# Kernel optimization log

Hardware: AMD Instinct MI355X
Metric: run time of the kernel (lower is better)

The kernel has to match this reference:

```python
import jax, jax.numpy as jnp
import numpy as np
import math

N, KZ, IFZ, AHZ, AFZ = 20000, 16, 256, 8, 32
EPS = 1e-5


def layernorm(x, g, b):
    m = jnp.mean(x, axis=-1, keepdims=True)
    v = jnp.mean((x - m) ** 2, axis=-1, keepdims=True)
    return (x - m) * jax.lax.rsqrt(v + EPS) * g + b


def rotate_half(x):
    x1, x2 = jnp.split(x, 2, axis=-1)
    return jnp.concatenate([-x2, x1], axis=-1)


def setup_inputs() -> dict:
    key = jax.random.key(0)
    ks = jax.random.split(key, 16)
    s = 1.0 / math.sqrt(IFZ)
    hf = AHZ * AFZ
    return {
        "x_1": jax.random.normal(ks[0], (N, IFZ), jnp.float32),
        "x_2": jax.random.normal(ks[1], (N, KZ, IFZ), jnp.float32),
        "pos_emb": jax.random.normal(ks[2], (N, AFZ), jnp.float32),
        "edge_index": jax.random.randint(ks[3], (N, KZ), 0, N),
        "Wq": jax.random.normal(ks[4], (IFZ, hf), jnp.float32) * s,
        "Wk": jax.random.normal(ks[5], (IFZ, hf), jnp.float32) * s,
        "Wv": jax.random.normal(ks[6], (IFZ, hf), jnp.float32) * s,
        "Wb": jax.random.normal(ks[7], (IFZ, AHZ), jnp.float32) * s,
        "bln_g": jnp.ones((IFZ,), jnp.float32),
        "bln_b": jnp.zeros((IFZ,), jnp.float32),
        "Wg": jax.random.normal(ks[8], (IFZ, hf), jnp.float32) * s,
        "bg": jnp.zeros((hf,), jnp.float32),
        "Wback": jax.random.normal(ks[9], (hf, IFZ), jnp.float32) / math.sqrt(hf),
        "bback": jnp.zeros((IFZ,), jnp.float32),
        "ln1_g": jnp.ones((IFZ,), jnp.float32),
        "ln1_b": jnp.zeros((IFZ,), jnp.float32),
    }


def reference(x_1, x_2, pos_emb, edge_index, Wq, Wk, Wv, Wb, bln_g, bln_b,
              Wg, bg, Wback, bback, ln1_g, ln1_b):
    n = x_1.shape[0]
    y_1 = x_1[edge_index]                                  # [N,kz,ifz] irregular gather
    q = (x_1 @ Wq).reshape(n, AHZ, AFZ)                    # [N,h,f]
    k = (y_1 @ Wk).reshape(n, KZ, AHZ, AFZ)                # [N,kz,h,f]
    # RoPE: rotate q by each node's own angles, k by gathered neighbor angles
    cos_q = jnp.cos(pos_emb)[:, None, :]                   # [N,1,f]
    sin_q = jnp.sin(pos_emb)[:, None, :]
    q = q * cos_q + rotate_half(q) * sin_q
    pe_n = pos_emb[edge_index]                             # [N,kz,f]
    cos_k = jnp.cos(pe_n)[:, :, None, :]                   # [N,kz,1,f]
    sin_k = jnp.sin(pe_n)[:, :, None, :]
    k = k * cos_k + rotate_half(k) * sin_k
    v = (y_1 @ Wv).reshape(n, KZ, AHZ, AFZ)
    bias_2 = layernorm(x_2, bln_g, bln_b) @ Wb             # [N,kz,h]
    gate = jax.nn.sigmoid(x_1 @ Wg + bg).reshape(n, AHZ, AFZ)
    scores = jnp.einsum('nhf,nkhf->nkh', q, k) / math.sqrt(AFZ) + bias_2
    w = jax.nn.softmax(scores, axis=1)                     # over kz neighbors
    out = gate * jnp.einsum('nkh,nkhf->nhf', w, v)         # [N,h,f]
    out = out.reshape(n, AHZ * AFZ) @ Wback + bback + math.sqrt(2.0) * x_1
    return layernorm(out, ln1_g, ln1_b)
```

## Files before the change

### kernel.cpp

```cpp
#include <hip/hip_runtime.h>
#include <math.h>

#define IFZ 256
#define KZ  16
#define AHZ 8
#define AFZ 32
#define HF  256

typedef _Float16 half8 __attribute__((ext_vector_type(8)));
typedef _Float16 half4 __attribute__((ext_vector_type(4)));
typedef float    f32x4 __attribute__((ext_vector_type(4)));

__global__ void conv_f16(const float* __restrict__ in, _Float16* __restrict__ out, int n4)
{
    int i = blockIdx.x * 256 + threadIdx.x;
    if (i >= n4) return;
    float4 v = reinterpret_cast<const float4*>(in)[i];
    half4 h;
    h[0] = (_Float16)v.x; h[1] = (_Float16)v.y;
    h[2] = (_Float16)v.z; h[3] = (_Float16)v.w;
    reinterpret_cast<half4*>(out)[i] = h;
}

__global__ void conv_wt(const float* __restrict__ w0, const float* __restrict__ w1,
                        const float* __restrict__ w2, const float* __restrict__ w3,
                        const float* __restrict__ w4, _Float16* __restrict__ out)
{
    int k = blockIdx.x;
    int m = blockIdx.y;
    int c = threadIdx.x;
    const float* w = (m == 0) ? w0 : (m == 1) ? w1 : (m == 2) ? w2 : (m == 3) ? w3 : w4;
    out[(size_t)m * 65536 + (size_t)c * 256 + k] = (_Float16)w[(size_t)k * 256 + c];
}

__global__ void prep_c1(const float* __restrict__ g, const float* __restrict__ b,
                        const float* __restrict__ Wb,
                        _Float16* __restrict__ c1T, float* __restrict__ c23)
{
    __shared__ float red[4][16];
    const int f = threadIdx.x;
    const int w = f >> 6, l = f & 63;
    const float gv = g[f], bv = b[f];
    float ph2[8], ph3[8];
    #pragma unroll
    for (int h = 0; h < 8; ++h) {
        float wv = Wb[(size_t)f * 8 + h];
        c1T[h * 256 + f] = (_Float16)(gv * wv);
        ph2[h] = gv * wv;
        ph3[h] = bv * wv;
    }
    c1T[8 * 256 + f] = (_Float16)1.0f;
    #pragma unroll
    for (int cc = 9; cc < 16; ++cc) c1T[cc * 256 + f] = (_Float16)0.0f;

    #pragma unroll
    for (int h = 0; h < 8; ++h) {
        #pragma unroll
        for (int o = 32; o > 0; o >>= 1) {
            ph2[h] += __shfl_xor(ph2[h], o);
            ph3[h] += __shfl_xor(ph3[h], o);
        }
        if (l == h) { red[w][h] = ph2[h]; red[w][8 + h] = ph3[h]; }
    }
    __syncthreads();
    if (f < 16) c23[f] = red[0][f] + red[1][f] + red[2][f] + red[3][f];
}

__launch_bounds__(256)
__global__ void gemm_qkvg(const _Float16* __restrict__ A, const _Float16* __restrict__ WT,
                          const float* __restrict__ pe, const float* __restrict__ bg,
                          _Float16* __restrict__ QH, _Float16* __restrict__ KH,
                          _Float16* __restrict__ VH, _Float16* __restrict__ GH, int N)
{
    __shared__ _Float16 as[64][40];
    __shared__ _Float16 bs[4][64][40];

    const int tid = threadIdx.x;
    const int l   = tid & 63;
    const int w   = tid >> 6;
    const int n0  = blockIdx.x * 64;
    const int c0  = blockIdx.y * 64;

    f32x4 acc[4][4];
    #pragma unroll
    for (int m = 0; m < 4; ++m)
        #pragma unroll
        for (int b = 0; b < 4; ++b)
            { acc[m][b][0]=0.f; acc[m][b][1]=0.f; acc[m][b][2]=0.f; acc[m][b][3]=0.f; }

    const int srow = tid >> 2;
    const int sch  = (tid & 3) * 8;
    const size_t aoff = (size_t)(n0 + srow) * IFZ + sch;
    const size_t boff = (size_t)(c0 + srow) * IFZ + sch;

    half8 av{}, bv0, bv1, bv2, bv3;
    if (n0 + srow < N) av = *reinterpret_cast<const half8*>(A + aoff);
    bv0 = *reinterpret_cast<const half8*>(WT + 0 * 65536 + boff);
    bv1 = *reinterpret_cast<const half8*>(WT + 1 * 65536 + boff);
    bv2 = *reinterpret_cast<const half8*>(WT + 2 * 65536 + boff);
    bv3 = *reinterpret_cast<const half8*>(WT + 3 * 65536 + boff);

    for (int kt = 0; kt < 8; ++kt) {
        __syncthreads();
        *reinterpret_cast<half8*>(&as[srow][sch])    = av;
        *reinterpret_cast<half8*>(&bs[0][srow][sch]) = bv0;
        *reinterpret_cast<half8*>(&bs[1][srow][sch]) = bv1;
        *reinterpret_cast<half8*>(&bs[2][srow][sch]) = bv2;
        *reinterpret_cast<half8*>(&bs[3][srow][sch]) = bv3;
        __syncthreads();

        half8 nav{}, nbv0{}, nbv1{}, nbv2{}, nbv3{};
        if (kt < 7) {
            const int k0 = (kt + 1) * 32;
            if (n0 + srow < N) nav = *reinterpret_cast<const half8*>(A + aoff + k0);
            nbv0 = *reinterpret_cast<const half8*>(WT + 0 * 65536 + boff + k0);
            nbv1 = *reinterpret_cast<const half8*>(WT + 1 * 65536 + boff + k0);
            nbv2 = *reinterpret_cast<const half8*>(WT + 2 * 65536 + boff + k0);
            nbv3 = *reinterpret_cast<const half8*>(WT + 3 * 65536 + boff + k0);
        }

        half8 af = *reinterpret_cast<const half8*>(&as[16 * w + (l & 15)][8 * (l >> 4)]);
        #pragma unroll
        for (int m = 0; m < 4; ++m) {
            #pragma unroll
            for (int b = 0; b < 4; ++b) {
                half8 bf = *reinterpret_cast<const half8*>(&bs[m][16 * b + (l & 15)][8 * (l >> 4)]);
                acc[m][b] = __builtin_amdgcn_mfma_f32_16x16x32_f16(af, bf, acc[m][b], 0, 0, 0);
            }
        }
        av = nav; bv0 = nbv0; bv1 = nbv1; bv2 = nbv2; bv3 = nbv3;
    }

    #pragma unroll
    for (int r = 0; r < 4; ++r) {
        const int grow = n0 + 16 * w + ((l >> 4) << 2) + r;
        if (grow >= N) continue;
        float a0 = pe[(size_t)grow * AFZ + (l & 15)];
        float a1 = pe[(size_t)grow * AFZ + 16 + (l & 15)];
        float s0, c0f, s1, c1f;
        __sincosf(a0, &s0, &c0f);
        __sincosf(a1, &s1, &c1f);
        #pragma unroll
        for (int m = 0; m < 2; ++m) {
            _Float16* o = m ? KH : QH;
            #pragma unroll
            for (int pb = 0; pb < 4; pb += 2) {
                float v0 = acc[m][pb][r], v1 = acc[m][pb + 1][r];
                o[(size_t)grow * HF + c0 + 16 * pb       + (l & 15)] = (_Float16)(v0 * c0f - v1 * s0);
                o[(size_t)grow * HF + c0 + 16 * (pb + 1) + (l & 15)] = (_Float16)(v1 * c1f + v0 * s1);
            }
        }
        #pragma unroll
        for (int b = 0; b < 4; ++b)
            VH[(size_t)grow * HF + c0 + 16 * b + (l & 15)] = (_Float16)acc[2][b][r];
        #pragma unroll
        for (int b = 0; b < 4; ++b) {
            const int c = c0 + 16 * b + (l & 15);
            float v = acc[3][b][r] + bg[c];
            GH[(size_t)grow * HF + c] = (_Float16)(1.f / (1.f + __expf(-v)));
        }
    }
}

__launch_bounds__(256)
__global__ void bias2_mfma(const float* __restrict__ x2,
                           const _Float16* __restrict__ c1T,
                           const float* __restrict__ c23,
                           float* __restrict__ out, int R)
{
    const int tid = threadIdx.x;
    const int l = tid & 63;
    const int w = tid >> 6;
    const int c = l & 15;
    const int p = l >> 4;

    const int R0 = (blockIdx.x * 4 + w) * 16;
    if (R0 >= R) return;

    const int arow = (R0 + c < R) ? (R0 + c) : (R - 1);
    const float* xr = x2 + (size_t)arow * IFZ + p * 8;

    f32x4 xv[16];
    #pragma unroll
    for (int kt = 0; kt < 8; ++kt) {
        xv[2 * kt]     = __builtin_nontemporal_load(reinterpret_cast<const f32x4*>(xr + kt * 32));
        xv[2 * kt + 1] = __builtin_nontemporal_load(reinterpret_cast<const f32x4*>(xr + kt * 32 + 4));
    }

    half8 bf[8];
    #pragma unroll
    for (int kt = 0; kt < 8; ++kt)
        bf[kt] = *reinterpret_cast<const half8*>(c1T + (size_t)c * 256 + kt * 32 + p * 8);

    f32x4 acc1 = {0.f, 0.f, 0.f, 0.f};
    f32x4 acc2 = {0.f, 0.f, 0.f, 0.f};
    #pragma unroll
    for (int kt = 0; kt < 8; ++kt) {
        f32x4 xa = xv[2 * kt], xb = xv[2 * kt + 1];
        half8 ax, ax2;
        ax[0] = (_Float16)xa[0]; ax[1] = (_Float16)xa[1];
        ax[2] = (_Float16)xa[2]; ax[3] = (_Float16)xa[3];
        ax[4] = (_Float16)xb[0]; ax[5] = (_Float16)xb[1];
        ax[6] = (_Float16)xb[2]; ax[7] = (_Float16)xb[3];
        ax2[0] = (_Float16)(xa[0] * xa[0]); ax2[1] = (_Float16)(xa[1] * xa[1]);
        ax2[2] = (_Float16)(xa[2] * xa[2]); ax2[3] = (_Float16)(xa[3] * xa[3]);
        ax2[4] = (_Float16)(xb[0] * xb[0]); ax2[5] = (_Float16)(xb[1] * xb[1]);
        ax2[6] = (_Float16)(xb[2] * xb[2]); ax2[7] = (_Float16)(xb[3] * xb[3]);
        acc1 = __builtin_amdgcn_mfma_f32_16x16x32_f16(ax,  bf[kt], acc1, 0, 0, 0);
        acc2 = __builtin_amdgcn_mfma_f32_16x16x32_f16(ax2, bf[kt], acc2, 0, 0, 0);
    }

    const float c2v = (c < 8) ? c23[c]     : 0.f;
    const float c3v = (c < 8) ? c23[8 + c] : 0.f;
    const int srcl = (l & 48) | 8;
    #pragma unroll
    for (int j = 0; j < 4; ++j) {
        float s1 = __shfl(acc1[j], srcl);
        float s2 = __shfl(acc2[j], srcl);
        float m    = s1 * (1.f / 256.f);
        float var  = s2 * (1.f / 256.f) - m * m;
        float rstd = rsqrtf(var + 1e-5f);
        const int row = R0 + 4 * p + j;
        if (c < 8 && row < R)
            out[(size_t)row * 8 + c] = rstd * (acc1[j] - m * c2v) + c3v;
    }
}

__launch_bounds__(256)
__global__ void attn_node(const _Float16* __restrict__ Qh, const _Float16* __restrict__ Kh,
                          const _Float16* __restrict__ Vh, const _Float16* __restrict__ Gh,
                          const int* __restrict__ eidx, const float* __restrict__ b2,
                          _Float16* __restrict__ AOh, int N)
{
    const int tid = threadIdx.x;
    const int l   = tid & 63;
    const int w   = tid >> 6;
    const int n   = blockIdx.x * 4 + w;
    if (n >= N) return;
    const int h = l >> 3;

    const int ei_reg = eidx[(size_t)n * KZ + (l & 15)];

    half4 qh4 = *reinterpret_cast<const half4*>(Qh + (size_t)n * HF + 4 * l);
    const float q0 = (float)qh4[0], q1 = (float)qh4[1],
                q2 = (float)qh4[2], q3 = (float)qh4[3];

    const float b2a = b2[(size_t)n * 128 + l];
    const float b2b = b2[(size_t)n * 128 + 64 + l];

    float sc[16];
    #pragma unroll
    for (int e = 0; e < 16; ++e) {
        const int row = __shfl(ei_reg, e);
        half4 kh4 = *reinterpret_cast<const half4*>(Kh + (size_t)row * HF + 4 * l);
        float s = q0 * (float)kh4[0] + q1 * (float)kh4[1]
                + q2 * (float)kh4[2] + q3 * (float)kh4[3];
        s += __shfl_xor(s, 1); s += __shfl_xor(s, 2); s += __shfl_xor(s, 4);
        sc[e] = s * 0.17677669529663687f;
    }
    #pragma unroll
    for (int e = 0; e < 8; ++e) sc[e]     += __shfl(b2a, e * 8 + h);
    #pragma unroll
    for (int e = 0; e < 8; ++e) sc[e + 8] += __shfl(b2b, e * 8 + h);

    float m = sc[0];
    #pragma unroll
    for (int e = 1; e < 16; ++e) m = fmaxf(m, sc[e]);
    float sum = 0.f;
    #pragma unroll
    for (int e = 0; e < 16; ++e) { sc[e] = __expf(sc[e] - m); sum += sc[e]; }
    const float inv = 1.f / sum;

    float o0 = 0.f, o1 = 0.f, o2 = 0.f, o3 = 0.f;
    #pragma unroll
    for (int e = 0; e < 16; ++e) {
        const int row = __shfl(ei_reg, e);
        half4 vh4 = *reinterpret_cast<const half4*>(Vh + (size_t)row * HF + 4 * l);
        const float we = sc[e] * inv;
        o0 = fmaf(we, (float)vh4[0], o0);
        o1 = fmaf(we, (float)vh4[1], o1);
        o2 = fmaf(we, (float)vh4[2], o2);
        o3 = fmaf(we, (float)vh4[3], o3);
    }

    half4 gh4 = *reinterpret_cast<const half4*>(Gh + (size_t)n * HF + 4 * l);
    half4 oh;
    oh[0] = (_Float16)(o0 * (float)gh4[0]);
    oh[1] = (_Float16)(o1 * (float)gh4[1]);
    oh[2] = (_Float16)(o2 * (float)gh4[2]);
    oh[3] = (_Float16)(o3 * (float)gh4[3]);
    *reinterpret_cast<half4*>(AOh + (size_t)n * HF + 4 * l) = oh;
}

__launch_bounds__(256)
__global__ void gemm_back(const _Float16* __restrict__ A, const _Float16* __restrict__ BT,
                          const float* __restrict__ bias, float* __restrict__ Y, int N)
{
    __shared__ _Float16 as[64][40];
    __shared__ _Float16 bs[64][40];

    const int tid = threadIdx.x;
    const int l   = tid & 63;
    const int w   = tid >> 6;
    const int n0  = blockIdx.x * 64;
    const int c0  = blockIdx.y * 64;

    f32x4 acc[4];
    #pragma unroll
    for (int b = 0; b < 4; ++b) { acc[b][0]=0.f; acc[b][1]=0.f; acc[b][2]=0.f; acc[b][3]=0.f; }

    const int srow = tid >> 2;
    const int sch  = (tid & 3) * 8;
    const size_t aoff = (size_t)(n0 + srow) * IFZ + sch;
    const size_t boff = (size_t)(c0 + srow) * IFZ + sch;

    half8 av{}, bv;
    if (n0 + srow < N) av = *reinterpret_cast<const half8*>(A + aoff);
    bv = *reinterpret_cast<const half8*>(BT + boff);

    for (int kt = 0; kt < 8; ++kt) {
        __syncthreads();
        *reinterpret_cast<half8*>(&as[srow][sch]) = av;
        *reinterpret_cast<half8*>(&bs[srow][sch]) = bv;
        __syncthreads();

        half8 nav{}, nbv{};
        if (kt < 7) {
            const int k0 = (kt + 1) * 32;
            if (n0 + srow < N) nav = *reinterpret_cast<const half8*>(A + aoff + k0);
            nbv = *reinterpret_cast<const half8*>(BT + boff + k0);
        }

        half8 af = *reinterpret_cast<const half8*>(&as[16 * w + (l & 15)][8 * (l >> 4)]);
        #pragma unroll
        for (int b = 0; b < 4; ++b) {
            half8 bf = *reinterpret_cast<const half8*>(&bs[16 * b + (l & 15)][8 * (l >> 4)]);
            acc[b] = __builtin_amdgcn_mfma_f32_16x16x32_f16(af, bf, acc[b], 0, 0, 0);
        }
        av = nav; bv = nbv;
    }

    #pragma unroll
    for (int r = 0; r < 4; ++r) {
        const int grow = n0 + 16 * w + ((l >> 4) << 2) + r;
        if (grow >= N) continue;
        #pragma unroll
        for (int b = 0; b < 4; ++b) {
            const int c = c0 + 16 * b + (l & 15);
            Y[(size_t)grow * HF + c] = acc[b][r] + bias[c];
        }
    }
}

__launch_bounds__(256)
__global__ void final_ln(const float* __restrict__ RAWb,
                         const float* __restrict__ x1b,
                         const float* __restrict__ g1,
                         const float* __restrict__ b1,
                         float* __restrict__ outb,
                         int N)
{
    int n    = blockIdx.x * 4 + (threadIdx.x >> 6);
    int lane = threadIdx.x & 63;
    if (n >= N) return;
    const size_t off = (size_t)n * IFZ + lane * 4;
    float4 ur = *reinterpret_cast<const float4*>(RAWb + off);
    float4 ux = *reinterpret_cast<const float4*>(x1b + off);
    float x[4];
    x[0] = ur.x + 1.4142135623730951f * ux.x;
    x[1] = ur.y + 1.4142135623730951f * ux.y;
    x[2] = ur.z + 1.4142135623730951f * ux.z;
    x[3] = ur.w + 1.4142135623730951f * ux.w;
    float s = x[0] + x[1] + x[2] + x[3];
    float q = x[0]*x[0] + x[1]*x[1] + x[2]*x[2] + x[3]*x[3];
    #pragma unroll
    for (int o = 32; o > 0; o >>= 1) { s += __shfl_xor(s, o); q += __shfl_xor(q, o); }
    float m    = s * (1.f / 256.f);
    float var  = q * (1.f / 256.f) - m * m;
    float rstd = rsqrtf(var + 1e-5f);
    float4 uo;
    {
        int f = lane * 4;
        uo.x = (x[0] - m) * rstd * g1[f + 0] + b1[f + 0];
        uo.y = (x[1] - m) * rstd * g1[f + 1] + b1[f + 1];
        uo.z = (x[2] - m) * rstd * g1[f + 2] + b1[f + 2];
        uo.w = (x[3] - m) * rstd * g1[f + 3] + b1[f + 3];
    }
    *reinterpret_cast<float4*>(outb + off) = uo;
}

extern "C" void kernel_launch(void* const* d_in, const int* in_sizes, int n_in,
                              void* d_out, int out_size, void* d_ws, size_t ws_size,
                              hipStream_t stream)
{
    const float* x1   = (const float*)d_in[0];
    const float* x2   = (const float*)d_in[1];
    const float* pe   = (const float*)d_in[2];
    const int*   ei   = (const int*)d_in[3];
    const float* wq   = (const float*)d_in[4];
    const float* wk   = (const float*)d_in[5];
    const float* wv   = (const float*)d_in[6];
    const float* wb   = (const float*)d_in[7];
    const float* blng = (const float*)d_in[8];
    const float* blnb = (const float*)d_in[9];
    const float* wg   = (const float*)d_in[10];
    const float* bg   = (const float*)d_in[11];
    const float* wbk  = (const float*)d_in[12];
    const float* bbk  = (const float*)d_in[13];
    const float* g1   = (const float*)d_in[14];
    const float* b1   = (const float*)d_in[15];

    const int N = in_sizes[0] / IFZ;

    const size_t S2 = (((size_t)N * HF * 2) + 4095) & ~(size_t)4095;
    char* base = (char*)d_ws;
    _Float16* X1H = (_Float16*)(base);
    _Float16* QH  = (_Float16*)(base + 1 * S2);
    _Float16* KH  = (_Float16*)(base + 2 * S2);
    _Float16* VH  = (_Float16*)(base + 3 * S2);
    _Float16* GH  = (_Float16*)(base + 4 * S2);
    float*    B2  = (float*)   (base + 5 * S2);
    _Float16* WT  = (_Float16*)(base + 6 * S2);
    _Float16* C1T = (_Float16*)(base + 6 * S2 + (1u << 20));
    float*    C23 = (float*)   (base + 6 * S2 + (1u << 20) + 8192);
    _Float16* AOH = QH;
    float*    RAW = (float*)(base + 2 * S2);

    conv_f16<<<dim3((N * IFZ / 4 + 255) / 256), 256, 0, stream>>>(x1, X1H, N * IFZ / 4);
    conv_wt<<<dim3(256, 5), 256, 0, stream>>>(wq, wk, wv, wg, wbk, WT);
    prep_c1<<<dim3(1), 256, 0, stream>>>(blng, blnb, wb, C1T, C23);

    const int nt = (N + 63) / 64;
    gemm_qkvg<<<dim3(nt, 4), 256, 0, stream>>>(X1H, WT, pe, bg, QH, KH, VH, GH, N);

    const int R = N * KZ;
    bias2_mfma<<<dim3((R + 63) / 64), 256, 0, stream>>>(x2, C1T, C23, B2, R);

    attn_node<<<dim3((N + 3) / 4), 256, 0, stream>>>(QH, KH, VH, GH, ei, B2, AOH, N);

    gemm_back<<<dim3(nt, 4), 256, 0, stream>>>(AOH, WT + 4 * 65536, bbk, RAW, N);

    final_ln<<<dim3((N + 3) / 4), 256, 0, stream>>>(RAW, x1, g1, b1, (float*)d_out, N);
}
```

Measured before the change: 188.7 us.

## Fuse bias_2 layernorm-projection into attention kernel and merge prep kernels

Computes the per-edge layernorm bias (x_2 projected by Wb via MFMA) inside the attention kernel, one wave per node covering its 16 edges, and hands the bias to the score computation through lane shuffles. This removes the B2 intermediate buffer round trip and one kernel launch. It also merges the weight transpose and the c1/c23 prep kernels into a single launch. In exchange the attention kernel carries more registers and has to stream x_2 (about 330MB) itself, which may lower occupancy and overlap.

```diff
diff --git a/kernel.cpp b/kernel.cpp
--- a/kernel.cpp
+++ b/kernel.cpp
@@ -22,21 +22,23 @@
     reinterpret_cast<half4*>(out)[i] = h;
 }
 
-__global__ void conv_wt(const float* __restrict__ w0, const float* __restrict__ w1,
-                        const float* __restrict__ w2, const float* __restrict__ w3,
-                        const float* __restrict__ w4, _Float16* __restrict__ out)
-{
-    int k = blockIdx.x;
-    int m = blockIdx.y;
-    int c = threadIdx.x;
-    const float* w = (m == 0) ? w0 : (m == 1) ? w1 : (m == 2) ? w2 : (m == 3) ? w3 : w4;
-    out[(size_t)m * 65536 + (size_t)c * 256 + k] = (_Float16)w[(size_t)k * 256 + c];
-}
-
-__global__ void prep_c1(const float* __restrict__ g, const float* __restrict__ b,
-                        const float* __restrict__ Wb,
-                        _Float16* __restrict__ c1T, float* __restrict__ c23)
-{
+__global__ void prep_all(const float* __restrict__ w0, const float* __restrict__ w1,
+                         const float* __restrict__ w2, const float* __restrict__ w3,
+                         const float* __restrict__ w4, _Float16* __restrict__ out,
+                         const float* __restrict__ g, const float* __restrict__ b,
+                         const float* __restrict__ Wb,
+                         _Float16* __restrict__ c1T, float* __restrict__ c23)
+{
+    const int m = blockIdx.y;
+    if (m < 5) {
+        int k = blockIdx.x;
+        int c = threadIdx.x;
+        const float* w = (m == 0) ? w0 : (m == 1) ? w1 : (m == 2) ? w2 : (m == 3) ? w3 : w4;
+        out[(size_t)m * 65536 + (size_t)c * 256 + k] = (_Float16)w[(size_t)k * 256 + c];
+        return;
+    }
+    if (blockIdx.x != 0) return;
+
     __shared__ float red[4][16];
     const int f = threadIdx.x;
     const int w = f >> 6, l = f & 63;
@@ -163,30 +165,30 @@
 }
 
 __launch_bounds__(256)
-__global__ void bias2_mfma(const float* __restrict__ x2,
-                           const _Float16* __restrict__ c1T,
-                           const float* __restrict__ c23,
-                           float* __restrict__ out, int R)
+__global__ void attn_fused(const _Float16* __restrict__ Qh, const _Float16* __restrict__ Kh,
+                           const _Float16* __restrict__ Vh, const _Float16* __restrict__ Gh,
+                           const int* __restrict__ eidx, const float* __restrict__ x2,
+                           const _Float16* __restrict__ c1T, const float* __restrict__ c23,
+                           _Float16* __restrict__ AOh, int N)
 {
     const int tid = threadIdx.x;
-    const int l = tid & 63;
-    const int w = tid >> 6;
+    const int l   = tid & 63;
+    const int w   = tid >> 6;
+    const int n   = blockIdx.x * 4 + w;
+    if (n >= N) return;
+    const int h = l >> 3;
     const int c = l & 15;
     const int p = l >> 4;
 
-    const int R0 = (blockIdx.x * 4 + w) * 16;
-    if (R0 >= R) return;
-
-    const int arow = (R0 + c < R) ? (R0 + c) : (R - 1);
-    const float* xr = x2 + (size_t)arow * IFZ + p * 8;
-
+    const int ei_reg = eidx[(size_t)n * KZ + c];
+
+    const float* xr = x2 + ((size_t)n * KZ + c) * IFZ + p * 8;
     f32x4 xv[16];
     #pragma unroll
     for (int kt = 0; kt < 8; ++kt) {
         xv[2 * kt]     = __builtin_nontemporal_load(reinterpret_cast<const f32x4*>(xr + kt * 32));
         xv[2 * kt + 1] = __builtin_nontemporal_load(reinterpret_cast<const f32x4*>(xr + kt * 32 + 4));
     }
-
     half8 bf[8];
     #pragma unroll
     for (int kt = 0; kt < 8; ++kt)
@@ -213,6 +215,7 @@
     const float c2v = (c < 8) ? c23[c]     : 0.f;
     const float c3v = (c < 8) ? c23[8 + c] : 0.f;
     const int srcl = (l & 48) | 8;
+    float bval[4];
     #pragma unroll
     for (int j = 0; j < 4; ++j) {
         float s1 = __shfl(acc1[j], srcl);
@@ -220,33 +223,12 @@
         float m    = s1 * (1.f / 256.f);
         float var  = s2 * (1.f / 256.f) - m * m;
         float rstd = rsqrtf(var + 1e-5f);
-        const int row = R0 + 4 * p + j;
-        if (c < 8 && row < R)
-            out[(size_t)row * 8 + c] = rstd * (acc1[j] - m * c2v) + c3v;
-    }
-}
-
-__launch_bounds__(256)
-__global__ void attn_node(const _Float16* __restrict__ Qh, const _Float16* __restrict__ Kh,
-                          const _Float16* __restrict__ Vh, const _Float16* __restrict__ Gh,
-                          const int* __restrict__ eidx, const float* __restrict__ b2,
-                          _Float16* __restrict__ AOh, int N)
-{
-    const int tid = threadIdx.x;
-    const int l   = tid & 63;
-    const int w   = tid >> 6;
-    const int n   = blockIdx.x * 4 + w;
-    if (n >= N) return;
-    const int h = l >> 3;
-
-    const int ei_reg = eidx[(size_t)n * KZ + (l & 15)];
+        bval[j] = rstd * (acc1[j] - m * c2v) + c3v;
+    }
 
     half4 qh4 = *reinterpret_cast<const half4*>(Qh + (size_t)n * HF + 4 * l);
     const float q0 = (float)qh4[0], q1 = (float)qh4[1],
                 q2 = (float)qh4[2], q3 = (float)qh4[3];
-
-    const float b2a = b2[(size_t)n * 128 + l];
-    const float b2b = b2[(size_t)n * 128 + 64 + l];
 
     float sc[16];
     #pragma unroll
@@ -256,12 +238,9 @@
         float s = q0 * (float)kh4[0] + q1 * (float)kh4[1]
                 + q2 * (float)kh4[2] + q3 * (float)kh4[3];
         s += __shfl_xor(s, 1); s += __shfl_xor(s, 2); s += __shfl_xor(s, 4);
-        sc[e] = s * 0.17677669529663687f;
-    }
-    #pragma unroll
-    for (int e = 0; e < 8; ++e) sc[e]     += __shfl(b2a, e * 8 + h);
-    #pragma unroll
-    for (int e = 0; e < 8; ++e) sc[e + 8] += __shfl(b2b, e * 8 + h);
+        sc[e] = s * 0.17677669529663687f
+              + __shfl(bval[e & 3], ((e >> 2) << 4) | h);
+    }
 
     float m = sc[0];
     #pragma unroll
@@ -419,24 +398,21 @@
     _Float16* KH  = (_Float16*)(base + 2 * S2);
     _Float16* VH  = (_Float16*)(base + 3 * S2);
     _Float16* GH  = (_Float16*)(base + 4 * S2);
-    float*    B2  = (float*)   (base + 5 * S2);
-    _Float16* WT  = (_Float16*)(base + 6 * S2);
-    _Float16* C1T = (_Float16*)(base + 6 * S2 + (1u << 20));
-    float*    C23 = (float*)   (base + 6 * S2 + (1u << 20) + 8192);
+    _Float16* WT  = (_Float16*)(base + 5 * S2);
+    _Float16* C1T = (_Float16*)(base + 5 * S2 + (1u << 20));
+    float*    C23 = (float*)   (base + 5 * S2 + (1u << 20) + 8192);
     _Float16* AOH = QH;
     float*    RAW = (float*)(base + 2 * S2);
 
     conv_f16<<<dim3((N * IFZ / 4 + 255) / 256), 256, 0, stream>>>(x1, X1H, N * IFZ / 4);
-    conv_wt<<<dim3(256, 5), 256, 0, stream>>>(wq, wk, wv, wg, wbk, WT);
-    prep_c1<<<dim3(1), 256, 0, stream>>>(blng, blnb, wb, C1T, C23);
+    prep_all<<<dim3(256, 6), 256, 0, stream>>>(wq, wk, wv, wg, wbk, WT,
+                                               blng, blnb, wb, C1T, C23);
 
     const int nt = (N + 63) / 64;
     gemm_qkvg<<<dim3(nt, 4), 256, 0, stream>>>(X1H, WT, pe, bg, QH, KH, VH, GH, N);
 
-    const int R = N * KZ;
-    bias2_mfma<<<dim3((R + 63) / 64), 256, 0, stream>>>(x2, C1T, C23, B2, R);
-
-    attn_node<<<dim3((N + 3) / 4), 256, 0, stream>>>(QH, KH, VH, GH, ei, B2, AOH, N);
+    attn_fused<<<dim3((N + 3) / 4), 256, 0, stream>>>(QH, KH, VH, GH, ei, x2,
+                                                      C1T, C23, AOH, N);
 
     gemm_back<<<dim3(nt, 4), 256, 0, stream>>>(AOH, WT + 4 * 65536, bbk, RAW, N);
 
```

Result: faster. 168.3 us (median of 2 runs) (-10.8%).
